# Performance work log

Hardware: AMD Instinct MI355X
Metric: run time of the kernel (lower is better)

## Reference

```python
import jax, jax.numpy as jnp
import numpy as np

N = 50000      # nodes
E = 400000     # edges
F = 64         # feature_size
H = 4          # heads
D = 16         # embedding_size (per-head dim)
HD = H * D     # concat hidden = 64
ED = 16        # edge_dim
L = 3          # model_layers (extra TransformerConv layers)
DN = 256       # dense_neurons
G = 128        # number of graphs in the batch
SCALE = float(1.0 / np.sqrt(D))


def setup_inputs() -> dict:
    key = jax.random.key(0)
    ks = jax.random.split(key, 40)

    def w(k, shape, fan_in):
        return jax.random.normal(k, shape, jnp.float32) / np.float32(np.sqrt(fan_in))

    inp = {}
    inp["x"] = jax.random.normal(ks[0], (N, F), jnp.float32)
    inp["edge_attr"] = jax.random.normal(ks[1], (E, ED), jnp.float32)
    inp["edge_index"] = jax.random.randint(ks[2], (2, E), 0, N)
    inp["batch"] = jnp.sort(jax.random.randint(ks[3], (N,), 0, G))

    # conv1: feature_size -> heads*embedding
    inp["Wq0"] = w(ks[4], (F, HD), F); inp["bq0"] = jnp.zeros((HD,), jnp.float32)
    inp["Wk0"] = w(ks[5], (F, HD), F); inp["bk0"] = jnp.zeros((HD,), jnp.float32)
    inp["Wv0"] = w(ks[6], (F, HD), F); inp["bv0"] = jnp.zeros((HD,), jnp.float32)
    inp["We0"] = w(ks[7], (ED, HD), ED)                      # lin_edge, no bias
    inp["Ws0"] = w(ks[8], (F, HD), F); inp["bs0"] = jnp.zeros((HD,), jnp.float32)  # lin_skip
    inp["Wb0"] = w(ks[9], (3 * HD, 1), 3 * HD)               # lin_beta, no bias

    # stacked layers 1..L: heads*embedding -> heads*embedding
    inp["Wq"] = w(ks[10], (L, HD, HD), HD); inp["bq"] = jnp.zeros((L, HD), jnp.float32)
    inp["Wk"] = w(ks[11], (L, HD, HD), HD); inp["bk"] = jnp.zeros((L, HD), jnp.float32)
    inp["Wv"] = w(ks[12], (L, HD, HD), HD); inp["bv"] = jnp.zeros((L, HD), jnp.float32)
    inp["We"] = w(ks[13], (L, ED, HD), ED)
    inp["Ws"] = w(ks[14], (L, HD, HD), HD); inp["bs"] = jnp.zeros((L, HD), jnp.float32)
    inp["Wb"] = w(ks[15], (L, 3 * HD, 1), 3 * HD)

    # MLP head: Linear(2*HD -> DN), Linear(DN -> 1)
    inp["Wlin"] = w(ks[16], (2 * HD, DN), 2 * HD); inp["blin"] = jnp.zeros((DN,), jnp.float32)
    inp["Wout"] = w(ks[17], (DN, 1), DN); inp["bout"] = jnp.zeros((1,), jnp.float32)
    return inp


def _tconv(x, edge_attr, src, dst, Wq, bq, Wk, bk, Wv, bv, We, Ws, bs, Wb):
    """PyG TransformerConv (concat=True, beta=True, edge_dim), eval mode (no dropout)."""
    n = x.shape[0]
    q = (x @ Wq + bq).reshape(n, H, D)
    k = (x @ Wk + bk).reshape(n, H, D)
    v = (x @ Wv + bv).reshape(n, H, D)
    e = (edge_attr @ We).reshape(-1, H, D)
    ke = k[src] + e                                   # [E,H,D] keys with edge feats
    ve = v[src] + e                                   # [E,H,D] values with edge feats
    logits = jnp.einsum('ehd,ehd->eh', q[dst], ke) * SCALE
    # segment softmax over incoming edges of each target node
    m = jax.ops.segment_max(logits, dst, num_segments=n)
    p = jnp.exp(logits - m[dst])
    s = jax.ops.segment_sum(p, dst, num_segments=n)
    a = p / (s[dst] + 1e-16)                          # [E,H]
    agg = jax.ops.segment_sum(a[:, :, None] * ve, dst, num_segments=n).reshape(n, HD)
    skip = x @ Ws + bs                                # root/skip transform
    beta = jax.nn.sigmoid(jnp.concatenate([agg, skip, agg - skip], axis=-1) @ Wb)
    return beta * skip + (1.0 - beta) * agg


def reference(x, edge_attr, edge_index, batch,
              Wq0, bq0, Wk0, bk0, Wv0, bv0, We0, Ws0, bs0, Wb0,
              Wq, bq, Wk, bk, Wv, bv, We, Ws, bs, Wb,
              Wlin, blin, Wout, bout):
    src, dst = edge_index[0], edge_index[1]
    h = jax.nn.relu(_tconv(x, edge_attr, src, dst,
                           Wq0, bq0, Wk0, bk0, Wv0, bv0, We0, Ws0, bs0, Wb0))
    for i in range(L):
        h = jax.nn.relu(_tconv(h, edge_attr, src, dst,
                               Wq[i], bq[i], Wk[i], bk[i], Wv[i], bv[i],
                               We[i], Ws[i], bs[i], Wb[i]))
    # global max pool (gmp) and global mean pool (gap)
    cnt = jax.ops.segment_sum(jnp.ones((h.shape[0],), h.dtype), batch, num_segments=G)
    gmax = jax.ops.segment_max(h, batch, num_segments=G)
    gmax = jnp.where(cnt[:, None] > 0, gmax, 0.0)
    gmean = jax.ops.segment_sum(h, batch, num_segments=G) / jnp.maximum(cnt[:, None], 1.0)
    z = jnp.concatenate([gmax, gmean], axis=-1) @ Wlin + blin
    return jax.nn.sigmoid(z @ Wout + bout)
```

## Files before the change

kernel.cpp:

```cpp
#include <hip/hip_runtime.h>
#include <math.h>

#define SCALEF 0.25f

typedef __attribute__((ext_vector_type(8))) short short8;
typedef __attribute__((ext_vector_type(4))) float f32x4;

__device__ __forceinline__ unsigned short f2bf(float x) {
  unsigned u = __float_as_uint(x);
  unsigned r = u + 0x7FFFu + ((u >> 16) & 1u);
  return (unsigned short)(r >> 16);
}
__device__ __forceinline__ float bf2f(unsigned short h) {
  return __uint_as_float(((unsigned)h) << 16);
}

__global__ void k_hist(const int* __restrict__ dst, int* __restrict__ counts, int E) {
  int i = blockIdx.x * 256 + threadIdx.x;
  if (i < E) atomicAdd(&counts[dst[i]], 1);
}

__global__ __launch_bounds__(1024) void k_scan1(const int* __restrict__ counts,
                                                int* __restrict__ excl,
                                                int* __restrict__ bsums, int n) {
  __shared__ int sd[1024];
  int t = threadIdx.x;
  int i = blockIdx.x * 1024 + t;
  int v = (i < n) ? counts[i] : 0;
  sd[t] = v;
  __syncthreads();
  for (int off = 1; off < 1024; off <<= 1) {
    int x = (t >= off) ? sd[t - off] : 0;
    __syncthreads();
    sd[t] += x;
    __syncthreads();
  }
  if (i < n) excl[i] = sd[t] - v;
  if (t == 1023) bsums[blockIdx.x] = sd[1023];
}

__global__ __launch_bounds__(64) void k_scan2(int* bsums, int nb) {
  const int lane = threadIdx.x;
  int v = (lane < nb) ? bsums[lane] : 0;
  const int orig = v;
  for (int off = 1; off < 64; off <<= 1) {
    int u = __shfl_up(v, off, 64);
    if (lane >= off) v += u;
  }
  if (lane < nb) bsums[lane] = v - orig;
}

__global__ __launch_bounds__(1024) void k_scan3(int* __restrict__ rowptr, int* __restrict__ cursor,
                                                const int* __restrict__ bsums, int n, int Etot) {
  int i = blockIdx.x * 1024 + threadIdx.x;
  if (i < n) { int v = rowptr[i] + bsums[blockIdx.x]; rowptr[i] = v; cursor[i] = v; }
  if (i == 0) rowptr[n] = Etot;
}

__global__ void k_scatperm(const int* __restrict__ esrc, const int* __restrict__ edst,
                           const float* __restrict__ EA, int* __restrict__ cursor,
                           int* __restrict__ esrcp, unsigned short* __restrict__ EAp, int E) {
  int i = blockIdx.x * 256 + threadIdx.x;
  if (i >= E) return;
  const int pos = atomicAdd(&cursor[edst[i]], 1);
  esrcp[pos] = esrc[i] * 256;
  const float4* s4 = (const float4*)(EA + ((size_t)i << 4));
  float4 a = s4[0], b = s4[1], c = s4[2], d = s4[3];
  union { unsigned short us[16]; uint4 u4[2]; } o;
  o.us[0] = f2bf(a.x); o.us[1] = f2bf(a.y); o.us[2] = f2bf(a.z); o.us[3] = f2bf(a.w);
  o.us[4] = f2bf(b.x); o.us[5] = f2bf(b.y); o.us[6] = f2bf(b.z); o.us[7] = f2bf(b.w);
  o.us[8] = f2bf(c.x); o.us[9] = f2bf(c.y); o.us[10] = f2bf(c.z); o.us[11] = f2bf(c.w);
  o.us[12] = f2bf(d.x); o.us[13] = f2bf(d.y); o.us[14] = f2bf(d.z); o.us[15] = f2bf(d.w);
  uint4* d4 = (uint4*)(EAp + ((size_t)pos << 4));
  d4[0] = o.u4[0]; d4[1] = o.u4[1];
}

__global__ __launch_bounds__(256) void k_wqt(
    const float* __restrict__ Wq0, const float* __restrict__ bq0, const float* __restrict__ We0,
    const float* __restrict__ Wq, const float* __restrict__ bq, const float* __restrict__ We,
    float* __restrict__ Wqt, float* __restrict__ bqt) {
  const int l = blockIdx.x;
  const float* wq = (l == 0) ? Wq0 : Wq + (l - 1) * 4096;
  const float* bv = (l == 0) ? bq0 : bq + (l - 1) * 64;
  const float* we = (l == 0) ? We0 : We + (l - 1) * 1024;
  float* out  = Wqt + l * 4096;
  float* outb = bqt + l * 64;
  const int t = threadIdx.x;
  const int r = t >> 2;
  const int hh = t & 3;
  float wqr[16];
  #pragma unroll
  for (int d = 0; d < 16; ++d) wqr[d] = wq[r * 64 + hh * 16 + d];
  #pragma unroll
  for (int bb = 0; bb < 16; ++bb) {
    float s = 0.f;
    #pragma unroll
    for (int d = 0; d < 16; ++d) s += wqr[d] * we[bb * 64 + hh * 16 + d];
    out[r * 64 + hh * 16 + bb] = s * SCALEF;
  }
  if (r == 0) {
    #pragma unroll
    for (int bb = 0; bb < 16; ++bb) {
      float s = 0.f;
      #pragma unroll
      for (int d = 0; d < 16; ++d) s += bv[hh * 16 + d] * we[bb * 64 + hh * 16 + d];
      outb[hh * 16 + bb] = s * SCALEF;
    }
  }
}

__global__ void k_prep(
    const float* __restrict__ x, unsigned short* __restrict__ xb, int n16,
    const float* __restrict__ Wq0, const float* __restrict__ Wk0, const float* __restrict__ Wv0,
    const float* __restrict__ Ws0,
    const float* __restrict__ Wq, const float* __restrict__ Wk, const float* __restrict__ Wv,
    const float* __restrict__ Ws, const float* __restrict__ Wqt,
    const float* __restrict__ bq0, const float* __restrict__ bk0, const float* __restrict__ bv0,
    const float* __restrict__ bs0,
    const float* __restrict__ bq, const float* __restrict__ bk, const float* __restrict__ bv,
    const float* __restrict__ bs, const float* __restrict__ bqt,
    unsigned short* __restrict__ WT, float* __restrict__ bcat) {
  const int id = blockIdx.x * 256 + threadIdx.x;
  if (id < n16) {
    float4 v = ((const float4*)x)[id];
    ushort4 o;
    o.x = f2bf(v.x); o.y = f2bf(v.y); o.z = f2bf(v.z); o.w = f2bf(v.w);
    ((ushort4*)xb)[id] = o;
  }
  if (id < 4 * 5 * 4096) {
    const int l = id / 20480;
    const int rem = id - l * 20480;
    const int mat = rem >> 12;
    const int idx = rem & 4095;
    const int k = idx >> 6;
    const int c = idx & 63;
    float v;
    if (mat == 0)      v = (l == 0) ? Wq0[idx] : Wq[(l - 1) * 4096 + idx];
    else if (mat == 1) v = (l == 0) ? Wk0[idx] : Wk[(l - 1) * 4096 + idx];
    else if (mat == 2) v = (l == 0) ? Wv0[idx] : Wv[(l - 1) * 4096 + idx];
    else if (mat == 3) v = (l == 0) ? Ws0[idx] : Ws[(l - 1) * 4096 + idx];
    else               v = Wqt[l * 4096 + idx];
    WT[(size_t)(l * 5 + mat) * 4096 + c * 64 + k] = f2bf(v);
    if (k == 0) {
      float b;
      if (mat == 0)      b = (l == 0) ? bq0[c] : bq[(l - 1) * 64 + c];
      else if (mat == 1) b = (l == 0) ? bk0[c] : bk[(l - 1) * 64 + c];
      else if (mat == 2) b = (l == 0) ? bv0[c] : bv[(l - 1) * 64 + c];
      else if (mat == 3) b = (l == 0) ? bs0[c] : bs[(l - 1) * 64 + c];
      else               b = bqt[l * 64 + c];
      bcat[(l * 5 + mat) * 64 + c] = b;
    }
  }
}

__global__ __launch_bounds__(256) void k_linm(
    const unsigned short* __restrict__ Xb, const unsigned short* __restrict__ WT,
    const float* __restrict__ bcat,
    unsigned short* __restrict__ Qb, unsigned short* __restrict__ KV16,
    unsigned short* __restrict__ Sb, unsigned short* __restrict__ Tb, int n) {
  const int lane = threadIdx.x & 63;
  const int tile = blockIdx.x * 4 + (threadIdx.x >> 6);
  const int ntr = n >> 4;
  if (tile >= ntr) return;
  const int r0 = tile << 4;
  const int c15 = lane & 15;
  const int kg = lane >> 4;
  const int rbase = r0 + kg * 4;

  const unsigned short* xrow = Xb + (size_t)(r0 + c15) * 64 + kg * 8;
  const short8 a0 = *(const short8*)(xrow);
  const short8 a1 = *(const short8*)(xrow + 32);

  #pragma unroll
  for (int mat = 0; mat < 5; ++mat) {
    const unsigned short* wb = WT + ((size_t)mat << 12) + (size_t)c15 * 64 + kg * 8;
    f32x4 acc0 = {0.f, 0.f, 0.f, 0.f}, acc1 = acc0, acc2 = acc0, acc3 = acc0;
    {
      short8 b0 = *(const short8*)(wb);
      short8 b1 = *(const short8*)(wb + 32);
      acc0 = __builtin_amdgcn_mfma_f32_16x16x32_bf16(a0, b0, acc0, 0, 0, 0);
      acc0 = __builtin_amdgcn_mfma_f32_16x16x32_bf16(a1, b1, acc0, 0, 0, 0);
    }
    {
      short8 b0 = *(const short8*)(wb + 16 * 64);
      short8 b1 = *(const short8*)(wb + 16 * 64 + 32);
      acc1 = __builtin_amdgcn_mfma_f32_16x16x32_bf16(a0, b0, acc1, 0, 0, 0);
      acc1 = __builtin_amdgcn_mfma_f32_16x16x32_bf16(a1, b1, acc1, 0, 0, 0);
    }
    {
      short8 b0 = *(const short8*)(wb + 32 * 64);
      short8 b1 = *(const short8*)(wb + 32 * 64 + 32);
      acc2 = __builtin_amdgcn_mfma_f32_16x16x32_bf16(a0, b0, acc2, 0, 0, 0);
      acc2 = __builtin_amdgcn_mfma_f32_16x16x32_bf16(a1, b1, acc2, 0, 0, 0);
    }
    {
      short8 b0 = *(const short8*)(wb + 48 * 64);
      short8 b1 = *(const short8*)(wb + 48 * 64 + 32);
      acc3 = __builtin_amdgcn_mfma_f32_16x16x32_bf16(a0, b0, acc3, 0, 0, 0);
      acc3 = __builtin_amdgcn_mfma_f32_16x16x32_bf16(a1, b1, acc3, 0, 0, 0);
    }

    const float* bb = bcat + mat * 64;
    const float bi0 = bb[c15], bi1 = bb[16 + c15], bi2 = bb[32 + c15], bi3 = bb[48 + c15];

    if (mat == 1 || mat == 2) {
      unsigned short* O = KV16 + (mat == 2 ? 1 : 0);
      #pragma unroll
      for (int reg = 0; reg < 4; ++reg) {
        const size_t ro = (size_t)(rbase + reg) * 128;
        O[ro + 2 * c15]        = f2bf(acc0[reg] + bi0);
        O[ro + 2 * (16 + c15)] = f2bf(acc1[reg] + bi1);
        O[ro + 2 * (32 + c15)] = f2bf(acc2[reg] + bi2);
        O[ro + 2 * (48 + c15)] = f2bf(acc3[reg] + bi3);
      }
    } else {
      unsigned short* O = (mat == 0) ? Qb : (mat == 3) ? Sb : Tb;
      #pragma unroll
      for (int reg = 0; reg < 4; ++reg) {
        const size_t ro = (size_t)(rbase + reg) * 64;
        O[ro + c15]      = f2bf(acc0[reg] + bi0);
        O[ro + 16 + c15] = f2bf(acc1[reg] + bi1);
        O[ro + 32 + c15] = f2bf(acc2[reg] + bi2);
        O[ro + 48 + c15] = f2bf(acc3[reg] + bi3);
      }
    }
  }
}

#define LOADST(KV, EE, jj) do {                                           \
    int jc_ = (jj) < mc ? (jj) : mc - 1;                                  \
    int off_ = __builtin_amdgcn_readlane(snv, jc_);                       \
    KV = *(const unsigned int*)(kvbase + off_);                           \
    EE = eabase[(size_t)(c0 + jc_) << 4];                                 \
  } while (0)

#define COMPUTE(KV, EE, jj) do {                                          \
    if ((jj) < mc) {                                                      \
      const float ef = bf2f(EE);                                          \
      const float kf = __uint_as_float(KV << 16);                         \
      const float vf = __uint_as_float(KV & 0xFFFF0000u);                 \
      float pl = qv * kf + tl * ef;                                       \
      pl += __shfl_xor(pl, 1, 64);                                        \
      pl += __shfl_xor(pl, 2, 64);                                        \
      pl += __shfl_xor(pl, 4, 64);                                        \
      pl += __shfl_xor(pl, 8, 64);                                        \
      const float p = __expf(pl);                                         \
      ssum += p;                                                          \
      accv += p * vf;                                                     \
      accw += p * ef;                                                     \
    }                                                                     \
  } while (0)

__global__ __launch_bounds__(128, 8) void k_attn(
    const unsigned short* __restrict__ Qb, const unsigned short* __restrict__ KV16,
    const unsigned short* __restrict__ Tb, const unsigned short* __restrict__ Sb,
    const unsigned short* __restrict__ EAp,
    const int* __restrict__ esrcp, const int* __restrict__ rowptr,
    const float* __restrict__ We, const float* __restrict__ Wb,
    unsigned short* __restrict__ Hout, int n) {
  const int t = threadIdx.x;
  const int lane = t & 63;
  const int node = blockIdx.x * 2 + (t >> 6);
  if (node >= n) return;

  const float qv = bf2f(Qb[(size_t)node * 64 + lane]) * SCALEF;
  const float tl = bf2f(Tb[(size_t)node * 64 + lane]);
  const int r0 = rowptr[node], r1 = rowptr[node + 1];

  const char* kvbase = (const char*)KV16 + 4 * lane;
  const unsigned short* eabase = EAp + (lane & 15);

  float ssum = 0.f, accv = 0.f, accw = 0.f;

  for (int c0 = r0; c0 < r1; c0 += 64) {
    const int mc = min(64, r1 - c0);
    int snv = 0;
    if (lane < mc) snv = esrcp[c0 + lane];

    unsigned int kvA, kvB, kvC, kvD;
    unsigned short eA, eB, eC, eD;
    LOADST(kvA, eA, 0);
    LOADST(kvB, eB, 1);
    LOADST(kvC, eC, 2);
    LOADST(kvD, eD, 3);

    for (int j = 0; j < mc; j += 4) {
      COMPUTE(kvA, eA, j);     LOADST(kvA, eA, j + 4);
      COMPUTE(kvB, eB, j + 1); LOADST(kvB, eB, j + 5);
      COMPUTE(kvC, eC, j + 2); LOADST(kvC, eC, j + 6);
      COMPUTE(kvD, eD, j + 3); LOADST(kvD, eD, j + 7);
    }
  }

  float agg = accv;
  #pragma unroll
  for (int j = 0; j < 16; ++j) {
    const float wj = __shfl(accw, (lane & 48) | j, 64);
    agg += wj * We[j * 64 + lane];
  }
  agg /= (ssum + 1e-16f);

  const float sk = bf2f(Sb[(size_t)node * 64 + lane]);
  float contrib = agg * Wb[lane] + sk * Wb[64 + lane] + (agg - sk) * Wb[128 + lane];
  #pragma unroll
  for (int off = 1; off < 64; off <<= 1) contrib += __shfl_xor(contrib, off, 64);
  const float beta = 1.f / (1.f + __expf(-contrib));
  const float o = beta * sk + (1.f - beta) * agg;
  Hout[(size_t)node * 64 + lane] = f2bf(fmaxf(o, 0.f));
}

__global__ __launch_bounds__(256) void k_poolmlp(const unsigned short* __restrict__ Hf,
    const int* __restrict__ batch,
    const float* __restrict__ Wlin, const float* __restrict__ blin,
    const float* __restrict__ Wout, const float* __restrict__ bout,
    float* __restrict__ out, int n) {
  const int g = blockIdx.x;
  const int t = threadIdx.x;
  const int lane = t & 63;
  const int w = t >> 6;

  int a = 0, b = n;
  while (a < b) { int mid = (a + b) >> 1; if (batch[mid] < g) a = mid + 1; else b = mid; }
  const int lo = a;
  b = n;
  while (a < b) { int mid = (a + b) >> 1; if (batch[mid] < g + 1) a = mid + 1; else b = mid; }
  const int hi = a;

  float vmax = -1e30f, vsum = 0.f;
  for (int i = lo + w; i < hi; i += 4) {
    const float v = bf2f(Hf[(size_t)i * 64 + lane]);
    vmax = fmaxf(vmax, v);
    vsum += v;
  }
  __shared__ float smax[4][64], ssum[4][64];
  __shared__ float cat[128];
  smax[w][lane] = vmax;
  ssum[w][lane] = vsum;
  __syncthreads();
  if (w == 0) {
    const float mx = fmaxf(fmaxf(smax[0][lane], smax[1][lane]),
                           fmaxf(smax[2][lane], smax[3][lane]));
    const float sm = ssum[0][lane] + ssum[1][lane] + ssum[2][lane] + ssum[3][lane];
    const int cnt = hi - lo;
    cat[lane]      = (cnt > 0) ? mx : 0.f;
    cat[64 + lane] = sm / fmaxf((float)cnt, 1.f);
  }
  __syncthreads();

  float acc = blin[t];
  for (int j = 0; j < 128; ++j) acc += cat[j] * Wlin[j * 256 + t];
  float p = acc * Wout[t];
  #pragma unroll
  for (int off = 1; off < 64; off <<= 1) p += __shfl_xor(p, off, 64);
  __shared__ float red[4];
  if ((t & 63) == 0) red[t >> 6] = p;
  __syncthreads();
  if (t == 0) {
    const float z = red[0] + red[1] + red[2] + red[3] + bout[0];
    out[g] = 1.f / (1.f + __expf(-z));
  }
}

extern "C" void kernel_launch(void* const* d_in, const int* in_sizes, int n_in,
                              void* d_out, int out_size, void* d_ws, size_t ws_size,
                              hipStream_t stream) {
  const float* x     = (const float*)d_in[0];
  const float* ea    = (const float*)d_in[1];
  const int*   eidx  = (const int*)d_in[2];
  const int*   batch = (const int*)d_in[3];
  const float *Wq0 = (const float*)d_in[4],  *bq0 = (const float*)d_in[5];
  const float *Wk0 = (const float*)d_in[6],  *bk0 = (const float*)d_in[7];
  const float *Wv0 = (const float*)d_in[8],  *bv0 = (const float*)d_in[9];
  const float *We0 = (const float*)d_in[10];
  const float *Ws0 = (const float*)d_in[11], *bs0 = (const float*)d_in[12];
  const float *Wb0 = (const float*)d_in[13];
  const float *Wq  = (const float*)d_in[14], *bq  = (const float*)d_in[15];
  const float *Wk  = (const float*)d_in[16], *bk  = (const float*)d_in[17];
  const float *Wv  = (const float*)d_in[18], *bv  = (const float*)d_in[19];
  const float *We  = (const float*)d_in[20];
  const float *Ws  = (const float*)d_in[21], *bs  = (const float*)d_in[22];
  const float *Wb  = (const float*)d_in[23];
  const float *Wlin = (const float*)d_in[24], *blin = (const float*)d_in[25];
  const float *Wout = (const float*)d_in[26], *bout = (const float*)d_in[27];

  const int N = in_sizes[0] / 64;
  const int E = in_sizes[2] / 2;
  const int G = out_size;
  const int* esrc = eidx;
  const int* edst = eidx + E;

  char* wsp = (char*)d_ws;
  auto alloc = [&](size_t bytes) -> void* {
    void* p = (void*)wsp;
    wsp += (bytes + 255) & ~(size_t)255;
    return p;
  };
  unsigned short* Qb = (unsigned short*)alloc((size_t)N * 64 * 2);
  unsigned short* KV16 = (unsigned short*)alloc((size_t)N * 64 * 4);
  unsigned short* Tb = (unsigned short*)alloc((size_t)N * 64 * 2);
  unsigned short* Sb16 = (unsigned short*)alloc((size_t)N * 64 * 2);
  unsigned short* Hb16 = (unsigned short*)alloc((size_t)N * 64 * 2);
  unsigned short* Xb16 = (unsigned short*)alloc((size_t)N * 64 * 2);
  int* counts  = (int*)alloc((size_t)N * 4);
  int* rowptr  = (int*)alloc((size_t)(N + 1) * 4);
  int* cursor  = (int*)alloc((size_t)N * 4);
  int* bsums   = (int*)alloc(1024 * 4);
  int* esrcp   = (int*)alloc((size_t)E * 4);
  unsigned short* EAp = (unsigned short*)alloc((size_t)E * 16 * 2);
  float* Wqt   = (float*)alloc(4 * 4096 * 4);
  float* bqt   = (float*)alloc(4 * 64 * 4);
  unsigned short* WT = (unsigned short*)alloc(4 * 5 * 4096 * 2);
  float* bcat  = (float*)alloc(4 * 5 * 64 * 4);

  const int gridE = (E + 255) / 256;
  const int NB1 = (N + 1023) / 1024;
  hipMemsetAsync(counts, 0, (size_t)N * 4, stream);
  k_hist<<<gridE, 256, 0, stream>>>(edst, counts, E);
  k_scan1<<<NB1, 1024, 0, stream>>>(counts, rowptr, bsums, N);
  k_scan2<<<1, 64, 0, stream>>>(bsums, NB1);
  k_scan3<<<NB1, 1024, 0, stream>>>(rowptr, cursor, bsums, N, E);
  k_scatperm<<<gridE, 256, 0, stream>>>(esrc, edst, ea, cursor, esrcp, EAp, E);
  k_wqt<<<4, 256, 0, stream>>>(Wq0, bq0, We0, Wq, bq, We, Wqt, bqt);
  k_prep<<<(N * 16 + 255) / 256, 256, 0, stream>>>(
      x, Xb16, N * 16,
      Wq0, Wk0, Wv0, Ws0, Wq, Wk, Wv, Ws, Wqt,
      bq0, bk0, bv0, bs0, bq, bk, bv, bs, bqt, WT, bcat);

  const int gridLinM = ((N >> 4) + 3) / 4;
  const int gridAttn = (N + 1) / 2;
  for (int l = 0; l < 4; ++l) {
    const float* we_ = (l == 0) ? We0 : We + (l - 1) * 1024;
    const float* wb_ = (l == 0) ? Wb0 : Wb + (l - 1) * 192;
    const unsigned short* xin = (l == 0) ? Xb16 : Hb16;
    k_linm<<<gridLinM, 256, 0, stream>>>(xin, WT + (size_t)l * 20480, bcat + l * 320,
                                         Qb, KV16, Sb16, Tb, N);
    k_attn<<<gridAttn, 128, 0, stream>>>(Qb, KV16, Tb, Sb16, EAp, esrcp, rowptr,
                                         we_, wb_, Hb16, N);
  }

  k_poolmlp<<<G, 256, 0, stream>>>(Hb16, batch, Wlin, blin, Wout, bout,
                                   (float*)d_out, N);
}
```

Baseline: 371.5 us.

## Merge scan kernels into one block and use DPP reduction with exp2

Replaces the three-kernel prefix scan with a single 1024-thread block in which each thread serially scans a contiguous chunk, removing two kernel launches. In the attention kernel, the shfl_xor butterfly reduction over 16 lanes becomes DPP row operations (quad permutes plus row shifts), and __expf becomes exp2f, with log2(e) folded into the query and edge-term scaling. The single-block scan reads counts with strided, uncoalesced access, and the DPP row-shift pattern must deliver the full 16-lane sum to every lane or the logits will be wrong.

```diff
diff --git a/kernel.cpp b/kernel.cpp
--- a/kernel.cpp
+++ b/kernel.cpp
@@ -2,6 +2,7 @@
 #include <math.h>
 
 #define SCALEF 0.25f
+#define LOG2E  1.4426950408889634f
 
 typedef __attribute__((ext_vector_type(8))) short short8;
 typedef __attribute__((ext_vector_type(4))) float f32x4;
@@ -20,14 +21,19 @@
   if (i < E) atomicAdd(&counts[dst[i]], 1);
 }
 
-__global__ __launch_bounds__(1024) void k_scan1(const int* __restrict__ counts,
-                                                int* __restrict__ excl,
-                                                int* __restrict__ bsums, int n) {
+__global__ __launch_bounds__(1024) void k_scanone(const int* __restrict__ counts,
+                                                  int* __restrict__ rowptr,
+                                                  int* __restrict__ cursor, int n, int E) {
   __shared__ int sd[1024];
-  int t = threadIdx.x;
-  int i = blockIdx.x * 1024 + t;
-  int v = (i < n) ? counts[i] : 0;
-  sd[t] = v;
+  const int t = threadIdx.x;
+  const int per = (n + 1023) >> 10;
+  const int base = t * per;
+  int s = 0;
+  for (int i = 0; i < per; ++i) {
+    const int idx = base + i;
+    if (idx < n) s += counts[idx];
+  }
+  sd[t] = s;
   __syncthreads();
   for (int off = 1; off < 1024; off <<= 1) {
     int x = (t >= off) ? sd[t - off] : 0;
@@ -35,26 +41,16 @@
     sd[t] += x;
     __syncthreads();
   }
-  if (i < n) excl[i] = sd[t] - v;
-  if (t == 1023) bsums[blockIdx.x] = sd[1023];
-}
-
-__global__ __launch_bounds__(64) void k_scan2(int* bsums, int nb) {
-  const int lane = threadIdx.x;
-  int v = (lane < nb) ? bsums[lane] : 0;
-  const int orig = v;
-  for (int off = 1; off < 64; off <<= 1) {
-    int u = __shfl_up(v, off, 64);
-    if (lane >= off) v += u;
-  }
-  if (lane < nb) bsums[lane] = v - orig;
-}
-
-__global__ __launch_bounds__(1024) void k_scan3(int* __restrict__ rowptr, int* __restrict__ cursor,
-                                                const int* __restrict__ bsums, int n, int Etot) {
-  int i = blockIdx.x * 1024 + threadIdx.x;
-  if (i < n) { int v = rowptr[i] + bsums[blockIdx.x]; rowptr[i] = v; cursor[i] = v; }
-  if (i == 0) rowptr[n] = Etot;
+  int run = (t == 0) ? 0 : sd[t - 1];
+  for (int i = 0; i < per; ++i) {
+    const int idx = base + i;
+    if (idx < n) {
+      rowptr[idx] = run;
+      cursor[idx] = run;
+      run += counts[idx];
+    }
+  }
+  if (t == 0) rowptr[n] = E;
 }
 
 __global__ void k_scatperm(const int* __restrict__ esrc, const int* __restrict__ edst,
@@ -227,6 +223,17 @@
   }
 }
 
+#define DPPRED(pl) do {                                                           \
+    pl += __int_as_float(__builtin_amdgcn_update_dpp(0, __float_as_int(pl),       \
+                                                     0xB1, 0xF, 0xF, true));      \
+    pl += __int_as_float(__builtin_amdgcn_update_dpp(0, __float_as_int(pl),       \
+                                                     0x4E, 0xF, 0xF, true));      \
+    pl += __int_as_float(__builtin_amdgcn_update_dpp(0, __float_as_int(pl),       \
+                                                     0x124, 0xF, 0xF, true));     \
+    pl += __int_as_float(__builtin_amdgcn_update_dpp(0, __float_as_int(pl),       \
+                                                     0x128, 0xF, 0xF, true));     \
+  } while (0)
+
 #define LOADST(KV, EE, jj) do {                                           \
     int jc_ = (jj) < mc ? (jj) : mc - 1;                                  \
     int off_ = __builtin_amdgcn_readlane(snv, jc_);                       \
@@ -240,11 +247,8 @@
       const float kf = __uint_as_float(KV << 16);                         \
       const float vf = __uint_as_float(KV & 0xFFFF0000u);                 \
       float pl = qv * kf + tl * ef;                                       \
-      pl += __shfl_xor(pl, 1, 64);                                        \
-      pl += __shfl_xor(pl, 2, 64);                                        \
-      pl += __shfl_xor(pl, 4, 64);                                        \
-      pl += __shfl_xor(pl, 8, 64);                                        \
-      const float p = __expf(pl);                                         \
+      DPPRED(pl);                                                         \
+      const float p = exp2f(pl);                                          \
       ssum += p;                                                          \
       accv += p * vf;                                                     \
       accw += p * ef;                                                     \
@@ -263,8 +267,8 @@
   const int node = blockIdx.x * 2 + (t >> 6);
   if (node >= n) return;
 
-  const float qv = bf2f(Qb[(size_t)node * 64 + lane]) * SCALEF;
-  const float tl = bf2f(Tb[(size_t)node * 64 + lane]);
+  const float qv = bf2f(Qb[(size_t)node * 64 + lane]) * (SCALEF * LOG2E);
+  const float tl = bf2f(Tb[(size_t)node * 64 + lane]) * LOG2E;
   const int r0 = rowptr[node], r1 = rowptr[node + 1];
 
   const char* kvbase = (const char*)KV16 + 4 * lane;
@@ -404,7 +408,6 @@
   int* counts  = (int*)alloc((size_t)N * 4);
   int* rowptr  = (int*)alloc((size_t)(N + 1) * 4);
   int* cursor  = (int*)alloc((size_t)N * 4);
-  int* bsums   = (int*)alloc(1024 * 4);
   int* esrcp   = (int*)alloc((size_t)E * 4);
   unsigned short* EAp = (unsigned short*)alloc((size_t)E * 16 * 2);
   float* Wqt   = (float*)alloc(4 * 4096 * 4);
@@ -413,12 +416,9 @@
   float* bcat  = (float*)alloc(4 * 5 * 64 * 4);
 
   const int gridE = (E + 255) / 256;
-  const int NB1 = (N + 1023) / 1024;
   hipMemsetAsync(counts, 0, (size_t)N * 4, stream);
   k_hist<<<gridE, 256, 0, stream>>>(edst, counts, E);
-  k_scan1<<<NB1, 1024, 0, stream>>>(counts, rowptr, bsums, N);
-  k_scan2<<<1, 64, 0, stream>>>(bsums, NB1);
-  k_scan3<<<NB1, 1024, 0, stream>>>(rowptr, cursor, bsums, N, E);
+  k_scanone<<<1, 1024, 0, stream>>>(counts, rowptr, cursor, N, E);
   k_scatperm<<<gridE, 256, 0, stream>>>(esrc, edst, ea, cursor, esrcp, EAp, E);
   k_wqt<<<4, 256, 0, stream>>>(Wq0, bq0, We0, Wq, bq, We, Wqt, bqt);
   k_prep<<<(N * 16 + 255) / 256, 256, 0, stream>>>(
```

Result: slower. 475.8 us (+28.1%).
